# Kernel optimization log

Hardware: AMD Instinct MI355X
Metric: run time of the kernel (lower is better)

Reference implementation:

```python
import jax, jax.numpy as jnp
import numpy as np

N_USER, N_MOVIE, E, H, L = 100000, 20000, 1000000, 64, 2
NEG_SLOPE = 0.2  # PyG GATv2Conv default negative_slope


def _rand_edges(k, n_src, n_dst, e):
    k1, k2 = jax.random.split(k)
    src = jax.random.randint(k1, (e,), 0, n_src, dtype=jnp.int32)
    dst = jax.random.randint(k2, (e,), 0, n_dst, dtype=jnp.int32)
    # ensure no src==dst index collisions so PyG's remove_self_loops is a no-op
    dst = jnp.where(dst == src, (dst + 1) % n_dst, dst)
    return jnp.stack([src, dst])


def setup_inputs() -> dict:
    key = jax.random.key(0)
    ks = jax.random.split(key, 8)
    return {
        "x_user": jax.random.normal(ks[0], (N_USER, H), jnp.float32),
        "x_movie": jax.random.normal(ks[1], (N_MOVIE, H), jnp.float32),
        "edge_u2m": _rand_edges(ks[2], N_USER, N_MOVIE, E),
        "edge_m2u": _rand_edges(ks[3], N_MOVIE, N_USER, E),
        # params stacked as [layer, edge_type, ...]; edge_type 0 = user->movie, 1 = movie->user
        "Wl": jax.random.normal(ks[4], (L, 2, H, H), jnp.float32) / np.sqrt(H).astype(np.float32),
        "bl": jnp.zeros((L, 2, H), jnp.float32),
        "Wr": jax.random.normal(ks[5], (L, 2, H, H), jnp.float32) / np.sqrt(H).astype(np.float32),
        "br": jnp.zeros((L, 2, H), jnp.float32),
        "att": jax.random.normal(ks[6], (L, 2, H), jnp.float32) / np.sqrt(H).astype(np.float32),
        "bias": jnp.zeros((L, 2, H), jnp.float32),
    }


def _segment_softmax(scores, seg, n):
    # numerically-stable softmax over variable-degree dst neighborhoods (PyG softmax)
    m = jax.ops.segment_max(scores, seg, num_segments=n)
    ex = jnp.exp(scores - m[seg])
    s = jax.ops.segment_sum(ex, seg, num_segments=n)
    return ex / (s[seg] + 1e-16)


def _gatv2(x_src, x_dst, edge, Wl, bl, Wr, br, att, bias):
    n_src, n_dst = x_src.shape[0], x_dst.shape[0]
    xl = x_src @ Wl + bl  # [N_src, H]
    xr = x_dst @ Wr + br  # [N_dst, H]
    n_loop = min(n_src, n_dst)  # PyG adds self loops with num_nodes = min(N_src, N_dst)
    loop = jnp.arange(n_loop, dtype=edge.dtype)
    src = jnp.concatenate([edge[0], loop])
    dst = jnp.concatenate([edge[1], loop])
    e = jax.nn.leaky_relu(xl[src] + xr[dst], NEG_SLOPE)  # [E', H] gathered per edge
    score = e @ att  # [E']
    alpha = _segment_softmax(score, dst, n_dst)
    out = jax.ops.segment_sum(xl[src] * alpha[:, None], dst, num_segments=n_dst)
    return out + bias


def reference(x_user, x_movie, edge_u2m, edge_m2u, Wl, bl, Wr, br, att, bias):
    for l in range(L):
        new_movie = _gatv2(x_user, x_movie, edge_u2m,
                           Wl[l, 0], bl[l, 0], Wr[l, 0], br[l, 0], att[l, 0], bias[l, 0])
        new_user = _gatv2(x_movie, x_user, edge_m2u,
                          Wl[l, 1], bl[l, 1], Wr[l, 1], br[l, 1], att[l, 1], bias[l, 1])
        x_movie = jax.nn.selu(new_movie)
        x_user = jax.nn.selu(new_user)
    return x_user, x_movie
```

## Files before the change

kernel.cpp:

```cpp
#include <hip/hip_runtime.h>
#include <hip/hip_fp16.h>
#include <cstdint>

#define H 64
#define EPR 16
#define NB 120

__device__ __forceinline__ float selu_f(float x) {
  const float sc = 1.0507009873554805f;
  const float al = 1.6732632423543772f;
  return x > 0.f ? sc * x : sc * al * (expf(x) - 1.f);
}

__global__ __launch_bounds__(256) void gemm64_dual2(
    const float* __restrict__ Au, const float* __restrict__ Am,
    const float* __restrict__ W0u, const float* __restrict__ b0u,
    const float* __restrict__ W1u, const float* __restrict__ b1u,
    const float* __restrict__ W0m, const float* __restrict__ b0m,
    const float* __restrict__ W1m, const float* __restrict__ b1m,
    __half* __restrict__ C0u, float* __restrict__ C1u,
    __half* __restrict__ C0m, float* __restrict__ C1m,
    int Nu, int Nm, int split) {
  __shared__ float Ws0[64 * 64];
  __shared__ float Ws1[64 * 64];
  __shared__ float As[64][65];
  __shared__ float bs0[64], bs1[64];

  const float *A, *W0, *b0, *W1, *b1;
  __half* C0; float* C1; int N, blk;
  if (blockIdx.x < split) {
    A = Au; W0 = W0u; b0 = b0u; W1 = W1u; b1 = b1u;
    C0 = C0u; C1 = C1u; N = Nu; blk = blockIdx.x;
  } else {
    A = Am; W0 = W0m; b0 = b0m; W1 = W1m; b1 = b1m;
    C0 = C0m; C1 = C1m; N = Nm; blk = blockIdx.x - split;
  }

  const int tid = threadIdx.x;
  for (int i = tid; i < 1024; i += 256) {
    ((float4*)Ws0)[i] = ((const float4*)W0)[i];
    ((float4*)Ws1)[i] = ((const float4*)W1)[i];
  }
  if (tid < 64) { bs0[tid] = b0[tid]; bs1[tid] = b1[tid]; }

  const int row0 = blk * 64;
  for (int i = tid; i < 1024; i += 256) {
    int r = i >> 4, c4 = i & 15;
    int row = row0 + r;
    float4 v = make_float4(0.f, 0.f, 0.f, 0.f);
    if (row < N) v = ((const float4*)(A + (size_t)row * H))[c4];
    As[r][c4 * 4 + 0] = v.x;
    As[r][c4 * 4 + 1] = v.y;
    As[r][c4 * 4 + 2] = v.z;
    As[r][c4 * 4 + 3] = v.w;
  }
  __syncthreads();

  const int g = tid & 3;
  const int r = tid >> 2;
  float a0[16], a1[16];
#pragma unroll
  for (int j = 0; j < 16; ++j) { a0[j] = bs0[g * 16 + j]; a1[j] = bs1[g * 16 + j]; }

  for (int k = 0; k < 64; ++k) {
    float ak = As[r][k];
    const float4* w0r = (const float4*)&Ws0[k * 64 + g * 16];
    const float4* w1r = (const float4*)&Ws1[k * 64 + g * 16];
#pragma unroll
    for (int j4 = 0; j4 < 4; ++j4) {
      float4 w0 = w0r[j4], w1 = w1r[j4];
      a0[j4 * 4 + 0] += ak * w0.x; a0[j4 * 4 + 1] += ak * w0.y;
      a0[j4 * 4 + 2] += ak * w0.z; a0[j4 * 4 + 3] += ak * w0.w;
      a1[j4 * 4 + 0] += ak * w1.x; a1[j4 * 4 + 1] += ak * w1.y;
      a1[j4 * 4 + 2] += ak * w1.z; a1[j4 * 4 + 3] += ak * w1.w;
    }
  }

  const int row = row0 + r;
  if (row < N) {
    unsigned pu[8];
#pragma unroll
    for (int j2 = 0; j2 < 8; ++j2) {
      __half2 t = __floats2half2_rn(a0[2 * j2], a0[2 * j2 + 1]);
      pu[j2] = *(unsigned*)&t;
    }
    uint4* c0 = (uint4*)(C0 + (size_t)row * H + g * 16);
    c0[0] = make_uint4(pu[0], pu[1], pu[2], pu[3]);
    c0[1] = make_uint4(pu[4], pu[5], pu[6], pu[7]);

    float4* c1 = (float4*)(C1 + (size_t)row * H + g * 16);
#pragma unroll
    for (int j4 = 0; j4 < 4; ++j4) {
      c1[j4] = make_float4(a1[j4 * 4 + 0], a1[j4 * 4 + 1], a1[j4 * 4 + 2], a1[j4 * 4 + 3]);
    }
  }
}

__global__ __launch_bounds__(256) void bucket_hist(
    const int* __restrict__ ed1, int E1r, int n1e, int sh1, int B1, int* __restrict__ mat1,
    const int* __restrict__ ed2, int E2r, int n2e, int sh2, int B2, int* __restrict__ mat2) {
  __shared__ int hist[256];
  int b = blockIdx.x;
  const int* ed; int Er, ne, sh, Bn, blk; int* mat;
  if (b < NB) { ed = ed1; Er = E1r; ne = n1e; sh = sh1; Bn = B1; mat = mat1; blk = b; }
  else { ed = ed2; Er = E2r; ne = n2e; sh = sh2; Bn = B2; mat = mat2; blk = b - NB; }
  for (int i = threadIdx.x; i < Bn; i += 256) hist[i] = 0;
  __syncthreads();
  int chunk = (ne + NB - 1) / NB;
  int lo = blk * chunk, hi = lo + chunk;
  if (hi > ne) hi = ne;
  for (int e = lo + threadIdx.x; e < hi; e += 256) {
    int d = (e < Er) ? ed[e] : (e - Er);
    atomicAdd(&hist[d >> sh], 1);
  }
  __syncthreads();
  for (int i = threadIdx.x; i < Bn; i += 256) mat[(size_t)i * NB + blk] = hist[i];
}

__global__ __launch_bounds__(256) void scan_partial2(
    const int* __restrict__ cnt1, int n1, int* __restrict__ psum1, int* __restrict__ bsum1,
    const int* __restrict__ cnt2, int n2, int* __restrict__ psum2, int* __restrict__ bsum2,
    int split) {
  __shared__ int sh[256];
  int b = blockIdx.x;
  const int* cnt; int n; int* psum; int* bsum; int lb;
  if (b < split) { cnt = cnt1; n = n1; psum = psum1; bsum = bsum1; lb = b; }
  else { cnt = cnt2; n = n2; psum = psum2; bsum = bsum2; lb = b - split; }
  int i = lb * 256 + threadIdx.x;
  int tid = threadIdx.x;
  sh[tid] = (i < n) ? cnt[i] : 0;
  __syncthreads();
  for (int off = 1; off < 256; off <<= 1) {
    int t = (tid >= off) ? sh[tid - off] : 0;
    __syncthreads();
    if (tid >= off) sh[tid] += t;
    __syncthreads();
  }
  if (i < n) psum[i] = sh[tid];
  if (tid == 255) bsum[lb] = sh[255];
}

__global__ __launch_bounds__(256) void scan_bsums2(
    int* __restrict__ bsum1, int nb1, int* __restrict__ bsum2, int nb2) {
  __shared__ int sh[256];
  const int tid = threadIdx.x;
  for (int which = 0; which < 2; ++which) {
    int* bsum = which ? bsum2 : bsum1;
    int nb = which ? nb2 : nb1;
    int run = 0;
    for (int start = 0; start < nb; start += 256) {
      int i = start + tid;
      int v = (i < nb) ? bsum[i] : 0;
      __syncthreads();
      sh[tid] = v;
      __syncthreads();
      for (int off = 1; off < 256; off <<= 1) {
        int t = (tid >= off) ? sh[tid - off] : 0;
        __syncthreads();
        if (tid >= off) sh[tid] += t;
        __syncthreads();
      }
      if (i < nb) bsum[i] = run + sh[tid] - v;
      run += sh[255];
      __syncthreads();
    }
  }
}

__global__ __launch_bounds__(256) void finalize_excl2(
    const int* __restrict__ cnt1, const int* __restrict__ psum1,
    const int* __restrict__ bsum1, int n1, int* __restrict__ excl1,
    const int* __restrict__ cnt2, const int* __restrict__ psum2,
    const int* __restrict__ bsum2, int n2, int* __restrict__ excl2, int split) {
  int b = blockIdx.x;
  const int *cnt, *psum, *bsum; int n; int* excl; int lb;
  if (b < split) { cnt = cnt1; psum = psum1; bsum = bsum1; n = n1; excl = excl1; lb = b; }
  else { cnt = cnt2; psum = psum2; bsum = bsum2; n = n2; excl = excl2; lb = b - split; }
  int i = lb * 256 + threadIdx.x;
  if (i >= n) return;
  excl[i] = psum[i] + bsum[lb] - cnt[i];
}

__global__ __launch_bounds__(256) void bucket_part(
    const int* __restrict__ es1, const int* __restrict__ ed1, int E1r, int n1e,
    int sh1, int B1, const int* __restrict__ excl1, unsigned* __restrict__ part1,
    const int* __restrict__ es2, const int* __restrict__ ed2, int E2r, int n2e,
    int sh2, int B2, const int* __restrict__ excl2, unsigned* __restrict__ part2) {
  __shared__ int cur[256];
  int b = blockIdx.x;
  const int *es, *ed, *excl; int Er, ne, sh, Bn, blk; unsigned* part;
  if (b < NB) { es = es1; ed = ed1; Er = E1r; ne = n1e; sh = sh1; Bn = B1; excl = excl1; part = part1; blk = b; }
  else { es = es2; ed = ed2; Er = E2r; ne = n2e; sh = sh2; Bn = B2; excl = excl2; part = part2; blk = b - NB; }
  for (int i = threadIdx.x; i < Bn; i += 256) cur[i] = excl[(size_t)i * NB + blk];
  __syncthreads();
  int chunk = (ne + NB - 1) / NB;
  int lo = blk * chunk, hi = lo + chunk;
  if (hi > ne) hi = ne;
  const unsigned lmask = (1u << sh) - 1u;
  for (int e = lo + threadIdx.x; e < hi; e += 256) {
    int s, d;
    if (e < Er) { s = es[e]; d = ed[e]; } else { s = e - Er; d = s; }
    int bkt = d >> sh;
    int pos = atomicAdd(&cur[bkt], 1);
    part[pos] = (((unsigned)d & lmask) << 18) | (unsigned)s;
  }
}

__global__ __launch_bounds__(256) void bucket_sort(
    const unsigned* __restrict__ part1, const int* __restrict__ excl1,
    int n1e, int sh1, int B1, int nd1, int* __restrict__ rp1, int* __restrict__ csr1,
    const unsigned* __restrict__ part2, const int* __restrict__ excl2,
    int n2e, int sh2, int B2, int nd2, int* __restrict__ rp2, int* __restrict__ csr2) {
  __shared__ int cnt_s[512];
  __shared__ int scan_s[512];
  int b = blockIdx.x;
  const unsigned* part; const int* excl; int ne, sh, Bn, nd, bkt; int *rp, *csr;
  if (b < B1) { part = part1; excl = excl1; ne = n1e; sh = sh1; Bn = B1; nd = nd1; rp = rp1; csr = csr1; bkt = b; }
  else { part = part2; excl = excl2; ne = n2e; sh = sh2; Bn = B2; nd = nd2; rp = rp2; csr = csr2; bkt = b - B1; }
  const int tid = threadIdx.x;
  const int dbase = bkt << sh;
  const int R = 1 << sh;
  int rcap = nd - dbase;
  if (rcap > R) rcap = R;
  const int base = excl[(size_t)bkt * NB];
  const int endv = (bkt == Bn - 1) ? ne : excl[(size_t)(bkt + 1) * NB];

  cnt_s[tid] = 0; cnt_s[256 + tid] = 0;
  __syncthreads();
  for (int i = base + tid; i < endv; i += 256)
    atomicAdd(&cnt_s[part[i] >> 18], 1);
  __syncthreads();
  scan_s[tid] = cnt_s[tid];
  scan_s[256 + tid] = cnt_s[256 + tid];
  __syncthreads();
  for (int off = 1; off < 256; off <<= 1) {
    int t = (tid >= off) ? scan_s[tid - off] : 0;
    __syncthreads();
    if (tid >= off) scan_s[tid] += t;
    __syncthreads();
  }
  for (int off = 1; off < 256; off <<= 1) {
    int t = (tid >= off) ? scan_s[256 + tid - off] : 0;
    __syncthreads();
    if (tid >= off) scan_s[256 + tid] += t;
    __syncthreads();
  }
  int lowtot = scan_s[255];
  scan_s[256 + tid] += lowtot;
  __syncthreads();
  if (tid < rcap) rp[dbase + tid + 1] = base + scan_s[tid];
  if (256 + tid < rcap) rp[dbase + 256 + tid + 1] = base + scan_s[256 + tid];
  cnt_s[tid] = base + scan_s[tid] - cnt_s[tid];
  cnt_s[256 + tid] = base + scan_s[256 + tid] - cnt_s[256 + tid];
  if (tid == 0 && bkt == 0) rp[0] = 0;
  __syncthreads();
  for (int i = base + tid; i < endv; i += 256) {
    unsigned p = part[i];
    int dl = p >> 18;
    int pos = atomicAdd(&cnt_s[dl], 1);
    csr[pos] = (int)(p & 0x3FFFFu);
  }
}

__global__ __launch_bounds__(256) void gat_dst2(
    const int* __restrict__ rp1, const int* __restrict__ csr1,
    const __half* __restrict__ xl1, const float* __restrict__ xr1,
    const float* __restrict__ att1, const float* __restrict__ bias1,
    float* __restrict__ out1, int nd1,
    const int* __restrict__ rp2, const int* __restrict__ csr2,
    const __half* __restrict__ xl2, const float* __restrict__ xr2,
    const float* __restrict__ att2, const float* __restrict__ bias2,
    float* __restrict__ out2, int nd2, int split) {
  __shared__ __align__(16) float tile[4][EPR * 64];

  const int b = blockIdx.x;
  const int* rp; const int* csr; const __half* xl; const float *xr, *att, *bias;
  float* out; int nd, d0;
  if (b < split) {
    rp = rp1; csr = csr1; xl = xl1; xr = xr1; att = att1; bias = bias1;
    out = out1; nd = nd1; d0 = b * 4;
  } else {
    rp = rp2; csr = csr2; xl = xl2; xr = xr2; att = att2; bias = bias2;
    out = out2; nd = nd2; d0 = (b - split) * 4;
  }
  const int w = threadIdx.x >> 6;
  const int d = d0 + w;
  if (d >= nd) return;
  const int h = threadIdx.x & 63;
  const unsigned h2 = (unsigned)h * 2u;
  const char* xlb = (const char*)xl;
  float* tl = tile[w];

  const float xr_h = xr[(size_t)d * H + h];
  const float a = att[h];
  const float a06 = 0.6f * a, a04 = 0.4f * a;
  const float bias_h = bias[h];
  const int beg = rp[d];
  const int end = rp[d + 1];

  const int r = h & 15;
  const int q = h >> 4;
  const int pr = (q << 2) ^ r;

  float o;

  if (end - beg <= EPR) {
    const int cnt = end - beg;
    float v[EPR];
#pragma unroll
    for (int qq = 0; qq < EPR / 4; ++qq) {
      if (qq * 4 < cnt) {
#pragma unroll
        for (int i = 0; i < 4; ++i) {
          const int k = qq * 4 + i;
          int j = k < cnt ? k : cnt - 1;
          unsigned src = (unsigned)csr[beg + j];
          v[k] = __half2float(*(const __half*)(xlb + ((src << 7) | h2)));
        }
      }
    }
#pragma unroll
    for (int qq = 0; qq < EPR / 4; ++qq) {
      if (qq * 4 < cnt) {
#pragma unroll
        for (int i = 0; i < 4; ++i) {
          const int k = qq * 4 + i;
          float p = v[k] + xr_h;
          tl[(k << 6) | (h ^ (k << 2))] = fmaf(p, a06, fabsf(p) * a04);
        }
      }
    }
    const float4* t4 = (const float4*)tl;
    float t0 = 0.f, t1 = 0.f, t2 = 0.f, t3 = 0.f;
#pragma unroll
    for (int c = 0; c < 4; ++c) {
      float4 q4 = t4[(r << 4) | (pr ^ c)];
      t0 += q4.x; t1 += q4.y; t2 += q4.z; t3 += q4.w;
    }
    float t = (t0 + t1) + (t2 + t3);
    t += __shfl_xor(t, 16, 64);
    t += __shfl_xor(t, 32, 64);
    t = (r < cnt) ? t : -3.0e38f;

    float M = t;
#pragma unroll
    for (int mk = 1; mk <= 8; mk <<= 1) M = fmaxf(M, __shfl_xor(M, mk, 64));
    float e = __expf(t - M);
    float S = e;
#pragma unroll
    for (int mk = 1; mk <= 8; mk <<= 1) S += __shfl_xor(S, mk, 64);
    if (h < 16) tl[h] = e;

    float P = 0.f;
#pragma unroll
    for (int qq = 0; qq < EPR / 4; ++qq) {
      if (qq * 4 < cnt) {
        float4 w4 = ((const float4*)tl)[qq];
        P += w4.x * v[qq * 4 + 0];
        P += w4.y * v[qq * 4 + 1];
        P += w4.z * v[qq * 4 + 2];
        P += w4.w * v[qq * 4 + 3];
      }
    }
    o = P / (S + 1e-16f) + bias_h;
  } else {
    float m = -3.0e38f, s = 0.f, acc = 0.f;
    int base = beg;
    float v[EPR], v2[EPR];

#pragma unroll
    for (int k = 0; k < EPR; ++k) {
      unsigned src = (unsigned)csr[base + k];
      v[k] = __half2float(*(const __half*)(xlb + ((src << 7) | h2)));
    }

    auto round = [&](float (&vc)[EPR], float (&vp)[EPR]) -> bool {
      int cnt = end - base;
      if (cnt > EPR) cnt = EPR;
#pragma unroll
      for (int qq = 0; qq < EPR / 4; ++qq) {
        if (qq * 4 < cnt) {
#pragma unroll
          for (int i = 0; i < 4; ++i) {
            const int k = qq * 4 + i;
            float p = vc[k] + xr_h;
            tl[(k << 6) | (h ^ (k << 2))] = fmaf(p, a06, fabsf(p) * a04);
          }
        }
      }
      const int nbase = base + EPR;
      int ncnt = end - nbase;
      const bool have_next = ncnt > 0;
      if (ncnt > EPR) ncnt = EPR;
      if (have_next) {
#pragma unroll
        for (int qq = 0; qq < EPR / 4; ++qq) {
          if (qq * 4 < ncnt) {
#pragma unroll
            for (int i = 0; i < 4; ++i) {
              const int k = qq * 4 + i;
              int j = k < ncnt ? k : ncnt - 1;
              unsigned src = (unsigned)csr[nbase + j];
              vp[k] = __half2float(*(const __half*)(xlb + ((src << 7) | h2)));
            }
          }
        }
      }
      const float4* t4 = (const float4*)tl;
      float t0 = 0.f, t1 = 0.f, t2 = 0.f, t3 = 0.f;
#pragma unroll
      for (int c = 0; c < 4; ++c) {
        float4 q4 = t4[(r << 4) | (pr ^ c)];
        t0 += q4.x; t1 += q4.y; t2 += q4.z; t3 += q4.w;
      }
      float t = (t0 + t1) + (t2 + t3);
      t += __shfl_xor(t, 16, 64);
      t += __shfl_xor(t, 32, 64);
      t = (r < cnt) ? t : -3.0e38f;

      float M = t;
#pragma unroll
      for (int mk = 1; mk <= 8; mk <<= 1) M = fmaxf(M, __shfl_xor(M, mk, 64));
      float e = __expf(t - M);
      float S = e;
#pragma unroll
      for (int mk = 1; mk <= 8; mk <<= 1) S += __shfl_xor(S, mk, 64);
      if (h < 16) tl[h] = e;

      float nm = fmaxf(m, M);
      float a_old = __expf(m - nm);
      float a_new = __expf(M - nm);
      float P = 0.f;
#pragma unroll
      for (int qq = 0; qq < EPR / 4; ++qq) {
        if (qq * 4 < cnt) {
          float4 w4 = ((const float4*)tl)[qq];
          P += w4.x * vc[qq * 4 + 0];
          P += w4.y * vc[qq * 4 + 1];
          P += w4.z * vc[qq * 4 + 2];
          P += w4.w * vc[qq * 4 + 3];
        }
      }
      s = s * a_old + S * a_new;
      acc = acc * a_old + P * a_new;
      m = nm;
      base = nbase;
      return have_next;
    };

    for (;;) {
      if (!round(v, v2)) break;
      if (!round(v2, v)) break;
    }
    o = acc / (s + 1e-16f) + bias_h;
  }

  out[(size_t)d * H + h] = selu_f(o);
}

extern "C" void kernel_launch(void* const* d_in, const int* in_sizes, int n_in,
                              void* d_out, int out_size, void* d_ws, size_t ws_size,
                              hipStream_t stream) {
  const float* x_user = (const float*)d_in[0];
  const float* x_movie = (const float*)d_in[1];
  const int* e_u2m = (const int*)d_in[2];
  const int* e_m2u = (const int*)d_in[3];
  const float* Wl = (const float*)d_in[4];
  const float* bl = (const float*)d_in[5];
  const float* Wr = (const float*)d_in[6];
  const float* br = (const float*)d_in[7];
  const float* att = (const float*)d_in[8];
  const float* bias = (const float*)d_in[9];

  const int n_user = in_sizes[0] / H;
  const int n_movie = in_sizes[1] / H;
  const int E1 = in_sizes[2] / 2;
  const int E2 = in_sizes[3] / 2;
  const int n_loop = n_user < n_movie ? n_user : n_movie;
  const int nE1 = E1 + n_loop;
  const int nE2 = E2 + n_loop;

  const int SHM = 7, SHU = 9;
  const int Bm = (n_movie + (1 << SHM) - 1) >> SHM;
  const int Bu = (n_user + (1 << SHU) - 1) >> SHU;
  const int nmatM = Bm * NB, nmatU = Bu * NB;
  const int nbm = (nmatM + 255) / 256, nbu = (nmatU + 255) / 256;

  float* ws = (float*)d_ws;
  size_t o = 0;
  __half* xl_u2m = (__half*)(ws + o); o += (size_t)n_user * H / 2;
  __half* xl_m2u = (__half*)(ws + o); o += (size_t)n_movie * H / 2;
  float* xr_u2m = ws + o; o += (size_t)n_movie * H;
  float* xr_m2u = ws + o; o += (size_t)n_user * H;

  int* matM  = (int*)(ws + o); o += nmatM;
  int* psumM = (int*)(ws + o); o += nmatM;
  int* exclM = (int*)(ws + o); o += nmatM;
  int* matU  = (int*)(ws + o); o += nmatU;
  int* psumU = (int*)(ws + o); o += nmatU;
  int* exclU = (int*)(ws + o); o += nmatU;
  int* bsumM = (int*)(ws + o); o += 1024;
  int* bsumU = (int*)(ws + o); o += 1024;
  unsigned* partM = (unsigned*)(ws + o); o += nE1;
  unsigned* partU = (unsigned*)(ws + o); o += nE2;
  int* csr1 = (int*)(ws + o); o += nE1;
  int* csr2 = (int*)(ws + o); o += nE2;
  int* rp1  = (int*)(ws + o); o += n_movie + 1;
  int* rp2  = (int*)(ws + o); o += n_user + 1;

  float* out_u = (float*)d_out;
  float* out_m = out_u + (size_t)n_user * H;

  const int gu = (n_user + 63) / 64;
  const int gm = (n_movie + 63) / 64;
  const int split1 = (n_movie + 3) / 4;
  const int split2 = (n_user + 3) / 4;

  bucket_hist<<<2 * NB, 256, 0, stream>>>(
      e_u2m + E1, E1, nE1, SHM, Bm, matM,
      e_m2u + E2, E2, nE2, SHU, Bu, matU);
  scan_partial2<<<nbm + nbu, 256, 0, stream>>>(
      matM, nmatM, psumM, bsumM, matU, nmatU, psumU, bsumU, nbm);
  scan_bsums2<<<1, 256, 0, stream>>>(bsumM, nbm, bsumU, nbu);
  finalize_excl2<<<nbm + nbu, 256, 0, stream>>>(
      matM, psumM, bsumM, nmatM, exclM,
      matU, psumU, bsumU, nmatU, exclU, nbm);
  bucket_part<<<2 * NB, 256, 0, stream>>>(
      e_u2m, e_u2m + E1, E1, nE1, SHM, Bm, exclM, partM,
      e_m2u, e_m2u + E2, E2, nE2, SHU, Bu, exclU, partU);
  bucket_sort<<<Bm + Bu, 256, 0, stream>>>(
      partM, exclM, nE1, SHM, Bm, n_movie, rp1, csr1,
      partU, exclU, nE2, SHU, Bu, n_user, rp2, csr2);

  for (int l = 0; l < 2; ++l) {
    const float* cu = (l == 0) ? x_user : out_u;
    const float* cm = (l == 0) ? x_movie : out_m;
    const int p0 = l * 2 + 0;
    const int p1 = l * 2 + 1;

    gemm64_dual2<<<gu + gm, 256, 0, stream>>>(
        cu, cm,
        Wl + (size_t)p0 * H * H, bl + (size_t)p0 * H,
        Wr + (size_t)p1 * H * H, br + (size_t)p1 * H,
        Wl + (size_t)p1 * H * H, bl + (size_t)p1 * H,
        Wr + (size_t)p0 * H * H, br + (size_t)p0 * H,
        xl_u2m, xr_m2u, xl_m2u, xr_u2m,
        n_user, n_movie, gu);

    gat_dst2<<<split1 + split2, 256, 0, stream>>>(
        rp1, csr1, xl_u2m, xr_u2m, att + (size_t)p0 * H, bias + (size_t)p0 * H,
        out_m, n_movie,
        rp2, csr2, xl_m2u, xr_m2u, att + (size_t)p1 * H, bias + (size_t)p1 * H,
        out_u, n_user, split1);
  }
}
```

Before: 482.8 us.

## Shrink CSR build buckets to fit one scan pass and uniformize row bounds

Bucket shift sizes drop from 7/9 to 5/8 bits, so the movie graph gets 625 buckets and the user graph 391. This raises the per-block histogram and cursor arrays to 640 entries and lets bucket_sort use a single 256-wide scan with no second half pass. The change trades more bucket_sort blocks and a larger partition matrix for less per-block serial scan work and better load balance. In gat_dst2, the row bounds are read through readfirstlane so the compiler treats them as wave-uniform and can use scalar loads for the CSR indices.

```diff
diff --git a/kernel.cpp b/kernel.cpp
--- a/kernel.cpp
+++ b/kernel.cpp
@@ -99,7 +99,7 @@
 __global__ __launch_bounds__(256) void bucket_hist(
     const int* __restrict__ ed1, int E1r, int n1e, int sh1, int B1, int* __restrict__ mat1,
     const int* __restrict__ ed2, int E2r, int n2e, int sh2, int B2, int* __restrict__ mat2) {
-  __shared__ int hist[256];
+  __shared__ int hist[640];
   int b = blockIdx.x;
   const int* ed; int Er, ne, sh, Bn, blk; int* mat;
   if (b < NB) { ed = ed1; Er = E1r; ne = n1e; sh = sh1; Bn = B1; mat = mat1; blk = b; }
@@ -186,7 +186,7 @@
     int sh1, int B1, const int* __restrict__ excl1, unsigned* __restrict__ part1,
     const int* __restrict__ es2, const int* __restrict__ ed2, int E2r, int n2e,
     int sh2, int B2, const int* __restrict__ excl2, unsigned* __restrict__ part2) {
-  __shared__ int cur[256];
+  __shared__ int cur[640];
   int b = blockIdx.x;
   const int *es, *ed, *excl; int Er, ne, sh, Bn, blk; unsigned* part;
   if (b < NB) { es = es1; ed = ed1; Er = E1r; ne = n1e; sh = sh1; Bn = B1; excl = excl1; part = part1; blk = b; }
@@ -211,8 +211,8 @@
     int n1e, int sh1, int B1, int nd1, int* __restrict__ rp1, int* __restrict__ csr1,
     const unsigned* __restrict__ part2, const int* __restrict__ excl2,
     int n2e, int sh2, int B2, int nd2, int* __restrict__ rp2, int* __restrict__ csr2) {
-  __shared__ int cnt_s[512];
-  __shared__ int scan_s[512];
+  __shared__ int cnt_s[256];
+  __shared__ int scan_s[256];
   int b = blockIdx.x;
   const unsigned* part; const int* excl; int ne, sh, Bn, nd, bkt; int *rp, *csr;
   if (b < B1) { part = part1; excl = excl1; ne = n1e; sh = sh1; Bn = B1; nd = nd1; rp = rp1; csr = csr1; bkt = b; }
@@ -225,13 +225,13 @@
   const int base = excl[(size_t)bkt * NB];
   const int endv = (bkt == Bn - 1) ? ne : excl[(size_t)(bkt + 1) * NB];
 
-  cnt_s[tid] = 0; cnt_s[256 + tid] = 0;
+  cnt_s[tid] = 0;
   __syncthreads();
   for (int i = base + tid; i < endv; i += 256)
     atomicAdd(&cnt_s[part[i] >> 18], 1);
   __syncthreads();
-  scan_s[tid] = cnt_s[tid];
-  scan_s[256 + tid] = cnt_s[256 + tid];
+  int c = cnt_s[tid];
+  scan_s[tid] = c;
   __syncthreads();
   for (int off = 1; off < 256; off <<= 1) {
     int t = (tid >= off) ? scan_s[tid - off] : 0;
@@ -239,19 +239,8 @@
     if (tid >= off) scan_s[tid] += t;
     __syncthreads();
   }
-  for (int off = 1; off < 256; off <<= 1) {
-    int t = (tid >= off) ? scan_s[256 + tid - off] : 0;
-    __syncthreads();
-    if (tid >= off) scan_s[256 + tid] += t;
-    __syncthreads();
-  }
-  int lowtot = scan_s[255];
-  scan_s[256 + tid] += lowtot;
-  __syncthreads();
   if (tid < rcap) rp[dbase + tid + 1] = base + scan_s[tid];
-  if (256 + tid < rcap) rp[dbase + 256 + tid + 1] = base + scan_s[256 + tid];
-  cnt_s[tid] = base + scan_s[tid] - cnt_s[tid];
-  cnt_s[256 + tid] = base + scan_s[256 + tid] - cnt_s[256 + tid];
+  cnt_s[tid] = base + scan_s[tid] - c;
   if (tid == 0 && bkt == 0) rp[0] = 0;
   __syncthreads();
   for (int i = base + tid; i < endv; i += 256) {
@@ -295,8 +284,8 @@
   const float a = att[h];
   const float a06 = 0.6f * a, a04 = 0.4f * a;
   const float bias_h = bias[h];
-  const int beg = rp[d];
-  const int end = rp[d + 1];
+  const int sbeg = __builtin_amdgcn_readfirstlane(rp[d]);
+  const int send = __builtin_amdgcn_readfirstlane(rp[d + 1]);
 
   const int r = h & 15;
   const int q = h >> 4;
@@ -304,8 +293,9 @@
 
   float o;
 
-  if (end - beg <= EPR) {
-    const int cnt = end - beg;
+  if (send - sbeg <= EPR) {
+    const int cnt = send - sbeg;
+    const int* csw = csr + sbeg;
     float v[EPR];
 #pragma unroll
     for (int qq = 0; qq < EPR / 4; ++qq) {
@@ -314,7 +304,7 @@
         for (int i = 0; i < 4; ++i) {
           const int k = qq * 4 + i;
           int j = k < cnt ? k : cnt - 1;
-          unsigned src = (unsigned)csr[beg + j];
+          unsigned src = (unsigned)csw[j];
           v[k] = __half2float(*(const __half*)(xlb + ((src << 7) | h2)));
         }
       }
@@ -365,17 +355,20 @@
     o = P / (S + 1e-16f) + bias_h;
   } else {
     float m = -3.0e38f, s = 0.f, acc = 0.f;
-    int base = beg;
+    int base = sbeg;
     float v[EPR], v2[EPR];
 
-#pragma unroll
-    for (int k = 0; k < EPR; ++k) {
-      unsigned src = (unsigned)csr[base + k];
-      v[k] = __half2float(*(const __half*)(xlb + ((src << 7) | h2)));
+    {
+      const int* csw = csr + base;
+#pragma unroll
+      for (int k = 0; k < EPR; ++k) {
+        unsigned src = (unsigned)csw[k];
+        v[k] = __half2float(*(const __half*)(xlb + ((src << 7) | h2)));
+      }
     }
 
     auto round = [&](float (&vc)[EPR], float (&vp)[EPR]) -> bool {
-      int cnt = end - base;
+      int cnt = send - base;
       if (cnt > EPR) cnt = EPR;
 #pragma unroll
       for (int qq = 0; qq < EPR / 4; ++qq) {
@@ -389,10 +382,11 @@
         }
       }
       const int nbase = base + EPR;
-      int ncnt = end - nbase;
+      int ncnt = send - nbase;
       const bool have_next = ncnt > 0;
       if (ncnt > EPR) ncnt = EPR;
       if (have_next) {
+        const int* csn = csr + nbase;
 #pragma unroll
         for (int qq = 0; qq < EPR / 4; ++qq) {
           if (qq * 4 < ncnt) {
@@ -400,7 +394,7 @@
             for (int i = 0; i < 4; ++i) {
               const int k = qq * 4 + i;
               int j = k < ncnt ? k : ncnt - 1;
-              unsigned src = (unsigned)csr[nbase + j];
+              unsigned src = (unsigned)csn[j];
               vp[k] = __half2float(*(const __half*)(xlb + ((src << 7) | h2)));
             }
           }
@@ -480,7 +474,7 @@
   const int nE1 = E1 + n_loop;
   const int nE2 = E2 + n_loop;
 
-  const int SHM = 7, SHU = 9;
+  const int SHM = 5, SHU = 8;
   const int Bm = (n_movie + (1 << SHM) - 1) >> SHM;
   const int Bu = (n_user + (1 << SHU) - 1) >> SHU;
   const int nmatM = Bm * NB, nmatU = Bu * NB;
```

After: 437.6 us. 1.1x faster.
